# Kernel optimization log

Hardware: AMD Instinct MI355X
Metric: run time of the kernel (lower is better)

## Reference

```python
import jax, jax.numpy as jnp
import numpy as np

DIM = 2048
N_HEADS = 32
N_KV_HEADS = 8
HEAD_DIM = DIM // N_HEADS
N_REP = N_HEADS // N_KV_HEADS
BSZ, SEQ = 2, 2048


def setup_inputs() -> dict:
    key = jax.random.key(0)
    ks = jax.random.split(key, 6)
    hidden_states = jax.random.normal(ks[0], (BSZ, SEQ, DIM), jnp.float32)
    # additive causal mask [1,1,S,S]
    causal = jnp.tril(jnp.ones((SEQ, SEQ), jnp.bool_))
    attention_mask = jnp.where(causal, 0.0, -1e9).astype(jnp.float32)[None, None]
    # RoPE tables [S, head_dim]
    inv_freq = 1.0 / (10000.0 ** (np.arange(0, HEAD_DIM, 2, dtype=np.float32) / HEAD_DIM))
    t = np.arange(SEQ, dtype=np.float32)
    freqs = np.outer(t, inv_freq)  # [S, head_dim/2]
    emb = np.concatenate([freqs, freqs], axis=-1)  # [S, head_dim]
    position_cos = jnp.asarray(np.cos(emb), jnp.float32)
    position_sin = jnp.asarray(np.sin(emb), jnp.float32)
    s = 0.02
    Wq = jax.random.normal(ks[1], (DIM, DIM), jnp.float32) * s
    Wk = jax.random.normal(ks[2], (N_KV_HEADS * HEAD_DIM, DIM), jnp.float32) * s
    Wv = jax.random.normal(ks[3], (N_KV_HEADS * HEAD_DIM, DIM), jnp.float32) * s
    Wo = jax.random.normal(ks[4], (DIM, DIM), jnp.float32) * s
    return {"hidden_states": hidden_states, "attention_mask": attention_mask,
            "position_cos": position_cos, "position_sin": position_sin,
            "Wq": Wq, "Wk": Wk, "Wv": Wv, "Wo": Wo}


def _rotate_half(x):
    x1, x2 = jnp.split(x, 2, axis=-1)
    return jnp.concatenate([-x2, x1], axis=-1)


def _apply_rope(x, cos, sin):
    # x: [b, h, s, d]; cos/sin: [s, d] broadcast over (b, h)
    return x * cos + _rotate_half(x) * sin


def reference(hidden_states, attention_mask, position_cos, position_sin, Wq, Wk, Wv, Wo):
    b, s, _ = hidden_states.shape
    q = jnp.einsum('bsd,ed->bse', hidden_states, Wq).reshape(b, s, N_HEADS, HEAD_DIM).transpose(0, 2, 1, 3)
    k = jnp.einsum('bsd,ed->bse', hidden_states, Wk).reshape(b, s, N_KV_HEADS, HEAD_DIM).transpose(0, 2, 1, 3)
    v = jnp.einsum('bsd,ed->bse', hidden_states, Wv).reshape(b, s, N_KV_HEADS, HEAD_DIM).transpose(0, 2, 1, 3)
    q = _apply_rope(q, position_cos, position_sin)
    k = _apply_rope(k, position_cos, position_sin)
    # GQA: group query heads over kv heads instead of physically repeating k/v
    qg = q.reshape(b, N_KV_HEADS, N_REP, s, HEAD_DIM)
    scores = jnp.einsum('bgrqd,bgkd->bgrqk', qg, k) * (1.0 / jnp.sqrt(jnp.float32(HEAD_DIM)))
    scores = scores + attention_mask[:, :, None, :s, :s]
    weights = jax.nn.softmax(scores.astype(jnp.float32), axis=-1).astype(q.dtype)
    attn = jnp.einsum('bgrqk,bgkd->bgrqd', weights, v)
    attn = attn.reshape(b, N_HEADS, s, HEAD_DIM).transpose(0, 2, 1, 3).reshape(b, s, DIM)
    out = jnp.einsum('bsd,ed->bse', attn, Wo)
    return out
```

## Files before the change

### kernel.cpp

```cpp
#include <hip/hip_runtime.h>
#include <math.h>

#define BSZ 2
#define SEQ 2048
#define DIM 2048
#define NH 32
#define NKV 8
#define HD 64
#define KVDIM 512

typedef short short8 __attribute__((ext_vector_type(8)));
typedef short short4v __attribute__((ext_vector_type(4)));
typedef float f32x4 __attribute__((ext_vector_type(4)));
typedef int i32x4 __attribute__((ext_vector_type(4)));

__device__ __forceinline__ short fbf(float x) {
    unsigned u = __float_as_uint(x);
    u = (u + 0x7fffu + ((u >> 16) & 1u)) >> 16;
    return (short)u;
}

#define AS1(p) ((const __attribute__((address_space(1))) void*)(p))
#define AS3(p) ((__attribute__((address_space(3))) void*)(p))

#if defined(__has_builtin)
#if __has_builtin(__builtin_amdgcn_permlane16_swap) && __has_builtin(__builtin_amdgcn_permlane32_swap)
#define HAVE_PERMLANE 1
#endif
#endif

__device__ __forceinline__ float redmax4(float x) {
#ifdef HAVE_PERMLANE
    {
        auto p = __builtin_amdgcn_permlane16_swap(__float_as_uint(x), __float_as_uint(x), false, false);
        x = fmaxf(__uint_as_float(p[0]), __uint_as_float(p[1]));
    }
    {
        auto p = __builtin_amdgcn_permlane32_swap(__float_as_uint(x), __float_as_uint(x), false, false);
        x = fmaxf(__uint_as_float(p[0]), __uint_as_float(p[1]));
    }
#else
    x = fmaxf(x, __shfl_xor(x, 16));
    x = fmaxf(x, __shfl_xor(x, 32));
#endif
    return x;
}
__device__ __forceinline__ float redsum4(float x) {
#ifdef HAVE_PERMLANE
    {
        auto p = __builtin_amdgcn_permlane16_swap(__float_as_uint(x), __float_as_uint(x), false, false);
        x = __uint_as_float(p[0]) + __uint_as_float(p[1]);
    }
    {
        auto p = __builtin_amdgcn_permlane32_swap(__float_as_uint(x), __float_as_uint(x), false, false);
        x = __uint_as_float(p[0]) + __uint_as_float(p[1]);
    }
#else
    x += __shfl_xor(x, 16);
    x += __shfl_xor(x, 32);
#endif
    return x;
}

__global__ __launch_bounds__(256) void prep(const float* __restrict__ X,
                                            const float* __restrict__ Wq,
                                            const float* __restrict__ Wk,
                                            const float* __restrict__ Wv,
                                            const float* __restrict__ Wo,
                                            short* __restrict__ Xb,
                                            short* __restrict__ Wqkv,
                                            short* __restrict__ Wob) {
    int i = blockIdx.x * 256 + threadIdx.x;
    const float* src; short* dst; int j;
    if (i < 2097152)      { src = X;  dst = Xb;             j = i; }
    else if (i < 3145728) { src = Wq; dst = Wqkv;           j = i - 2097152; }
    else if (i < 3407872) { src = Wk; dst = Wqkv + 4194304; j = i - 3145728; }
    else if (i < 3670016) { src = Wv; dst = Wqkv + 5242880; j = i - 3407872; }
    else                  { src = Wo; dst = Wob;            j = i - 3670016; }
    float4 f = ((const float4*)src)[j];
    short4v s = { fbf(f.x), fbf(f.y), fbf(f.z), fbf(f.w) };
    ((short4v*)dst)[j] = s;
}

__global__ __launch_bounds__(512, 2) void gemm_qkv(const short* __restrict__ A,
                                                   const short* __restrict__ W,
                                                   const float* __restrict__ cosT,
                                                   const float* __restrict__ sinT,
                                                   short* __restrict__ Qo,
                                                   short* __restrict__ Ko,
                                                   short* __restrict__ Vo) {
    __shared__ short SM[65536];
    const int K = 2048;
    const int NT = 64;
    const int tid = threadIdx.x;
    const int lane = tid & 63, wave = tid >> 6;
    const int l15 = lane & 15, quad = lane >> 4;
    const int wm = (wave >> 2) * 128;
    const int wn = (wave & 3) * 64;
    const int orig = blockIdx.x;
    const int wgid = (orig & 7) * 24 + (orig >> 3);
    const int by = wgid / 12, bx = wgid - by * 12;
    const int m0 = by * 256, n0 = bx * 256;

    size_t aoff[2], boff[2]; int lslot[2];
#pragma unroll
    for (int v = 0; v < 2; ++v) {
        int s = v * 512 + tid;
        int pr = s >> 3, w = s & 7;
        int row = (pr << 1) | (w & 1);
        int c = (w >> 1) ^ (pr & 3);
        aoff[v] = (size_t)(m0 + row) * K + c * 8;
        boff[v] = (size_t)(n0 + row) * K + c * 8;
        lslot[v] = s * 8;
    }
    const int r0a = wm + l15;
    const int pa = r0a >> 1;
    const int slotA0 = pa * 8 + (((quad ^ (pa & 3)) << 1) | (r0a & 1));
    const int r0b = wn + l15;
    const int pb = r0b >> 1;
    const int slotB0 = pb * 8 + (((quad ^ (pb & 3)) << 1) | (r0b & 1));

    f32x4 acc[8][4] = {};

    auto issue = [&](int t) {
        const int kb = t * 32;
        short* Ad = SM + (t & 3) * 8192;
        short* Bd = SM + 32768 + (t & 3) * 8192;
#pragma unroll
        for (int v = 0; v < 2; ++v) {
            __builtin_amdgcn_global_load_lds(AS1(A + aoff[v] + kb), AS3(Ad + lslot[v]), 16, 0, 0);
            __builtin_amdgcn_global_load_lds(AS1(W + boff[v] + kb), AS3(Bd + lslot[v]), 16, 0, 0);
        }
    };
    issue(0); issue(1); issue(2);
    asm volatile("s_waitcnt vmcnt(8)" ::: "memory");
    __builtin_amdgcn_s_barrier();
    asm volatile("" ::: "memory");
    __builtin_amdgcn_sched_barrier(0);

    for (int t = 0; t < NT; ++t) {
        if (t < NT - 3) issue(t + 3);
        const short* Ab = SM + (t & 3) * 8192;
        const short* Bb = SM + 32768 + (t & 3) * 8192;
        short8 af[8], bf8[4];
#pragma unroll
        for (int j = 0; j < 4; ++j)
            bf8[j] = *(const short8*)&Bb[(slotB0 + j * 64) * 8];
#pragma unroll
        for (int i = 0; i < 8; ++i)
            af[i] = *(const short8*)&Ab[(slotA0 + i * 64) * 8];
        __builtin_amdgcn_s_setprio(1);
#pragma unroll
        for (int i = 0; i < 8; ++i)
#pragma unroll
            for (int j = 0; j < 4; ++j)
                acc[i][j] = __builtin_amdgcn_mfma_f32_16x16x32_bf16(af[i], bf8[j], acc[i][j], 0, 0, 0);
        __builtin_amdgcn_s_setprio(0);
        if (t < NT - 3)       asm volatile("s_waitcnt vmcnt(8)" ::: "memory");
        else if (t == NT - 3) asm volatile("s_waitcnt vmcnt(4)" ::: "memory");
        else if (t == NT - 2) asm volatile("s_waitcnt vmcnt(0)" ::: "memory");
        __builtin_amdgcn_s_barrier();
        asm volatile("" ::: "memory");
        __builtin_amdgcn_sched_barrier(0);
    }

    const int n0r = n0 + wn;
    if (n0r < 2560) {
        short* dst; int heads, hh; float scale;
        if (n0r < 2048) { dst = Qo; heads = NH;  hh = n0r >> 6;          scale = 0.125f * 1.44269504088896f; }
        else            { dst = Ko; heads = NKV; hh = (n0r - 2048) >> 6; scale = 1.0f; }
        short* EB = SM + wave * 8192;
#pragma unroll
        for (int i = 0; i < 8; ++i)
#pragma unroll
            for (int r = 0; r < 4; ++r) {
                int rr = i * 16 + quad * 4 + r;
                int s = (m0 + wm + rr) & (SEQ - 1);
                int msk = ((rr >> 1) & 7) * 8;
#pragma unroll
                for (int jp = 0; jp < 2; ++jp) {
                    int d1 = jp * 16 + l15;
                    float c1 = cosT[s * HD + d1], s1v = sinT[s * HD + d1];
                    float x1 = acc[i][jp][r], x2 = acc[i][jp + 2][r];
                    EB[rr * 64 + (d1 ^ msk)]        = fbf((x1 * c1 - x2 * s1v) * scale);
                    EB[rr * 64 + ((d1 + 32) ^ msk)] = fbf((x2 * c1 + x1 * s1v) * scale);
                }
            }
#pragma unroll
        for (int t = 0; t < 16; ++t) {
            int rr = (lane >> 3) + t * 8;
            int c = lane & 7;
            short8 v8 = *(const short8*)&EB[rr * 64 + c * 8];
            int dchunk = c ^ ((rr >> 1) & 7);
            int mrow = m0 + wm + rr;
            int s = mrow & (SEQ - 1), bb = mrow >> 11;
            *(short8*)&dst[((size_t)(bb * SEQ + s) * heads + hh) * HD + dchunk * 8] = v8;
        }
    } else {
        const int hh = (n0r - 2560) >> 6;
#pragma unroll
        for (int i = 0; i < 8; ++i) {
            int mrow4 = m0 + wm + i * 16 + quad * 4;
            int s_abs = mrow4 & (SEQ - 1);
            int bb = mrow4 >> 11;
            int blk = s_abs >> 6, kk = s_abs & 63;
            int ob = ((kk >> 5) << 3) | (((kk >> 2) & 3) << 1) | ((kk >> 4) & 1);
#pragma unroll
            for (int j = 0; j < 4; ++j) {
                int d = j * 16 + l15;
                short4v pk = { fbf(acc[i][j][0]), fbf(acc[i][j][1]),
                               fbf(acc[i][j][2]), fbf(acc[i][j][3]) };
                *(short4v*)&Vo[(((size_t)(bb * NKV + hh) * HD + d) * SEQ) + blk * 64 + ob * 4] = pk;
            }
        }
    }
}

__global__ __launch_bounds__(256) void gemm_bf16(const short* __restrict__ A,
                                                 const short* __restrict__ W,
                                                 float* __restrict__ C,
                                                 int M, int N, int K) {
    __shared__ short As[128 * 64];
    __shared__ short Bs[128 * 64];
    const int tid = threadIdx.x;
    const int lane = tid & 63, wave = tid >> 6;
    const int l15 = lane & 15, quad = lane >> 4;
    const int m0 = blockIdx.y * 128, n0 = blockIdx.x * 128;
    const int wm = (wave >> 1) * 64, wn = (wave & 1) * 64;
    f32x4 acc[4][4] = {};
    int srow[4], gcol[4];
#pragma unroll
    for (int v = 0; v < 4; ++v) {
        int s = v * 256 + tid;
        srow[v] = s >> 3;
        gcol[v] = ((s & 7) ^ (srow[v] & 7)) * 8;
    }
    for (int kb = 0; kb < K; kb += 64) {
        __syncthreads();
#pragma unroll
        for (int v = 0; v < 4; ++v) {
            int s = v * 256 + tid;
            __builtin_amdgcn_global_load_lds(AS1(A + (size_t)(m0 + srow[v]) * K + kb + gcol[v]),
                                             AS3(&As[s * 8]), 16, 0, 0);
            __builtin_amdgcn_global_load_lds(AS1(W + (size_t)(n0 + srow[v]) * K + kb + gcol[v]),
                                             AS3(&Bs[s * 8]), 16, 0, 0);
        }
        __syncthreads();
#pragma unroll
        for (int kh = 0; kh < 2; ++kh) {
            const int cs = ((kh * 4 + quad) ^ (l15 & 7)) * 8;
            short8 af[4], bf8[4];
#pragma unroll
            for (int i = 0; i < 4; ++i)
                af[i] = *(const short8*)&As[(wm + i * 16 + l15) * 64 + cs];
#pragma unroll
            for (int j = 0; j < 4; ++j)
                bf8[j] = *(const short8*)&Bs[(wn + j * 16 + l15) * 64 + cs];
#pragma unroll
            for (int i = 0; i < 4; ++i)
#pragma unroll
                for (int j = 0; j < 4; ++j)
                    acc[i][j] = __builtin_amdgcn_mfma_f32_16x16x32_bf16(af[i], bf8[j], acc[i][j], 0, 0, 0);
        }
    }
#pragma unroll
    for (int i = 0; i < 4; ++i)
#pragma unroll
        for (int j = 0; j < 4; ++j)
#pragma unroll
            for (int r = 0; r < 4; ++r)
                C[(size_t)(m0 + wm + i * 16 + quad * 4 + r) * N + n0 + wn + j * 16 + l15] = acc[i][j][r];
}

__global__ __launch_bounds__(512, 4) void flash4(const short* __restrict__ Qb,
                                                 const short* __restrict__ Kb,
                                                 const short* __restrict__ VT,
                                                 short* __restrict__ O) {
    __shared__ short Ks[2][128 * 64];
    __shared__ short Vs[2][64 * 128];
    const int d = blockIdx.x + blockIdx.y * 64;
    const int bh = (d & 255) >> 2;
    const int qt = (d < 256) ? 7 - (d & 3) : (d & 3);
    const int b = bh >> 5, h = bh & 31, kvh = h >> 2;
    const int tid = threadIdx.x;
    const int wave = tid >> 6, lane = tid & 63;
    const int l15 = lane & 15, quad = lane >> 4;

    short8 qf[2][2];
#pragma unroll
    for (int g = 0; g < 2; ++g) {
        const short* qp = Qb + ((size_t)b * SEQ + qt * 256 + g * 128 + wave * 16 + l15) * DIM + h * HD + quad * 8;
        qf[g][0] = *(const short8*)qp;
        qf[g][1] = *(const short8*)(qp + 32);
    }
    f32x4 o[2][4] = {};
    float m[2] = {-1e30f, -1e30f}, l[2] = {0.f, 0.f};

    const short* Kbase = Kb + (size_t)b * SEQ * KVDIM + kvh * HD;
    const short* Vbase = VT + (size_t)(b * NKV + kvh) * HD * SEQ;

    int krow[2], kcol[2], vrow[2], vcol[2];
#pragma unroll
    for (int v = 0; v < 2; ++v) {
        int s = v * 512 + tid;
        krow[v] = s >> 3;
        kcol[v] = ((s & 7) ^ (krow[v] & 7)) * 8;
        vrow[v] = s >> 4;
        vcol[v] = ((s & 15) ^ (vrow[v] & 7)) * 8;
    }
    auto issue = [&](int kt, int bi) {
#pragma unroll
        for (int v = 0; v < 2; ++v) {
            int s = v * 512 + tid;
            __builtin_amdgcn_global_load_lds(AS1(Kbase + (size_t)(kt * 128 + krow[v]) * KVDIM + kcol[v]),
                                             AS3(&Ks[bi][s * 8]), 16, 0, 0);
            __builtin_amdgcn_global_load_lds(AS1(Vbase + (size_t)vrow[v] * SEQ + kt * 128 + vcol[v]),
                                             AS3(&Vs[bi][s * 8]), 16, 0, 0);
        }
    };
    issue(0, 0);
    const int nkt = 2 * qt + 2;
    for (int kt = 0; kt < nkt; ++kt) {
        const int bi = kt & 1;
        __syncthreads();
        if (kt + 1 < nkt) issue(kt + 1, bi ^ 1);

#pragma unroll
        for (int g = 0; g < 2; ++g) {
            const int qmin = qt * 256 + g * 128 + wave * 16;
            if (kt * 128 > qmin + 15) continue;
            f32x4 st[8] = {};
#pragma unroll
            for (int kh = 0; kh < 2; ++kh) {
                const int cs = ((kh * 4 + quad) ^ (l15 & 7)) * 8;
#pragma unroll
                for (int nt = 0; nt < 8; ++nt) {
                    short8 ka = *(const short8*)&Ks[bi][(nt * 16 + l15) * 64 + cs];
                    st[nt] = __builtin_amdgcn_mfma_f32_16x16x32_bf16(ka, qf[g][kh], st[nt], 0, 0, 0);
                }
            }
            if (kt * 128 + 127 > qmin) {
                const int q = qmin + l15;
#pragma unroll
                for (int nt = 0; nt < 8; ++nt)
                    if (kt * 128 + nt * 16 + 15 > qmin) {
#pragma unroll
                        for (int r = 0; r < 4; ++r)
                            if (kt * 128 + nt * 16 + quad * 4 + r > q) st[nt][r] = -1e30f;
                    }
            }
            float mnt[8];
#pragma unroll
            for (int nt = 0; nt < 8; ++nt)
                mnt[nt] = fmaxf(fmaxf(fmaxf(st[nt][0], st[nt][1]), st[nt][2]), st[nt][3]);
            float ma = fmaxf(fmaxf(mnt[0], mnt[1]), mnt[2]);
            float mb = fmaxf(fmaxf(mnt[3], mnt[4]), mnt[5]);
            float mc = fmaxf(fmaxf(mnt[6], mnt[7]), ma);
            float mx = redmax4(fmaxf(mb, mc));

            const bool noskip = !__all(mx <= m[g]);
            float mn = m[g];
            float al = 1.0f;
            float alr[4];
            if (noskip) {
                mn = fmaxf(m[g], mx);
                al = __builtin_amdgcn_exp2f(m[g] - mn);
                m[g] = mn;
#pragma unroll
                for (int r = 0; r < 4; ++r) alr[r] = __shfl(al, quad * 4 + r);
            }
            i32x4 aw[4];
            f32x4 rs4 = {};
#pragma unroll
            for (int nt = 0; nt < 8; ++nt) {
                f32x4 pv;
#pragma unroll
                for (int r = 0; r < 4; ++r) pv[r] = __builtin_amdgcn_exp2f(st[nt][r] - mn);
                rs4 += pv;
                unsigned u0 = __float_as_uint(pv[0]) + 0x8000u;
                unsigned u1 = __float_as_uint(pv[1]) + 0x8000u;
                unsigned u2 = __float_as_uint(pv[2]) + 0x8000u;
                unsigned u3 = __float_as_uint(pv[3]) + 0x8000u;
                aw[nt >> 1][(nt & 1) * 2 + 0] = (int)__builtin_amdgcn_perm(u1, u0, 0x07060302u);
                aw[nt >> 1][(nt & 1) * 2 + 1] = (int)__builtin_amdgcn_perm(u3, u2, 0x07060302u);
            }
            float rs = redsum4((rs4[0] + rs4[1]) + (rs4[2] + rs4[3]));
            l[g] = l[g] * al + rs;
            if (noskip) {
#pragma unroll
                for (int dt = 0; dt < 4; ++dt) {
                    o[g][dt][0] *= alr[0]; o[g][dt][1] *= alr[1];
                    o[g][dt][2] *= alr[2]; o[g][dt][3] *= alr[3];
                }
            }
#pragma unroll
            for (int dt = 0; dt < 4; ++dt) {
                f32x4 t = o[g][dt];
#pragma unroll
                for (int kh = 0; kh < 4; ++kh) {
                    const int slot = (kh * 4 + quad) ^ (l15 & 7);
                    short8 vf = *(const short8*)&Vs[bi][(dt * 16 + l15) * 128 + slot * 8];
                    t = __builtin_amdgcn_mfma_f32_16x16x32_bf16(__builtin_bit_cast(short8, aw[kh]), vf, t, 0, 0, 0);
                }
                o[g][dt] = t;
            }
        }
    }
#pragma unroll
    for (int g = 0; g < 2; ++g) {
        float li = 1.0f / l[g];
        float lr[4];
#pragma unroll
        for (int r = 0; r < 4; ++r) lr[r] = __shfl(li, quad * 4 + r);
        short* Oo = O + ((size_t)b * SEQ + qt * 256 + g * 128 + wave * 16 + quad * 4) * DIM + h * HD + l15;
#pragma unroll
        for (int r = 0; r < 4; ++r)
#pragma unroll
            for (int dt = 0; dt < 4; ++dt)
                Oo[(size_t)r * DIM + dt * 16] = fbf(o[g][dt][r] * lr[r]);
    }
}

extern "C" void kernel_launch(void* const* d_in, const int* in_sizes, int n_in,
                              void* d_out, int out_size, void* d_ws, size_t ws_size,
                              hipStream_t stream) {
    const float* X    = (const float*)d_in[0];
    const float* cosT = (const float*)d_in[2];
    const float* sinT = (const float*)d_in[3];
    const float* Wq   = (const float*)d_in[4];
    const float* Wk   = (const float*)d_in[5];
    const float* Wv   = (const float*)d_in[6];
    const float* Wo   = (const float*)d_in[7];

    char* ws = (char*)d_ws;
    short* Xb    = (short*)(ws);
    short* ATTb  = Xb;
    short* WQKVb = (short*)(ws + 16777216);
    short* Wob   = (short*)(ws + 29360128);
    short* Qbb   = (short*)(ws + 37748736);
    short* Kbb   = (short*)(ws + 54525952);
    short* VTb   = (short*)(ws + 58720256);

    const int M = BSZ * SEQ;
    dim3 blk(256);

    prep<<<dim3(18432), blk, 0, stream>>>(X, Wq, Wk, Wv, Wo, Xb, WQKVb, Wob);
    gemm_qkv<<<dim3(192), dim3(512), 0, stream>>>(Xb, WQKVb, cosT, sinT, Qbb, Kbb, VTb);
    flash4<<<dim3(64, 8), dim3(512), 0, stream>>>(Qbb, Kbb, VTb, ATTb);
    gemm_bf16<<<dim3(DIM / 128, M / 128), blk, 0, stream>>>(ATTb, Wob, (float*)d_out, M, DIM, DIM);
}
```

Measured before the change: 307.5 us.

## Pipeline output GEMM with 4-stage LDS ring and shrink flash attention tiles

The output-projection GEMM now runs 512 threads on 256x128 tiles. It uses a 4-deep ring of K=32 LDS buffers with explicit vmcnt waits, a single barrier per step, setprio around the MFMA blocks, and a remapped workgroup id for L2 locality. The flash attention kernel drops to 128 query rows and 64-key tiles per block, which doubles the grid to 1024 blocks. It also swaps __syncthreads for manual barriers and waitcnts and adds setprio. The goal is to hide global load latency and improve load balance, at the cost of more blocks that each reload the K/V tiles and hand-tuned waitcnt accounting.

```diff
diff --git a/kernel.cpp b/kernel.cpp
--- a/kernel.cpp
+++ b/kernel.cpp
@@ -216,52 +216,89 @@
     }
 }
 
-__global__ __launch_bounds__(256) void gemm_bf16(const short* __restrict__ A,
-                                                 const short* __restrict__ W,
-                                                 float* __restrict__ C,
-                                                 int M, int N, int K) {
-    __shared__ short As[128 * 64];
-    __shared__ short Bs[128 * 64];
+__global__ __launch_bounds__(512, 2) void gemm_bf16(const short* __restrict__ A,
+                                                    const short* __restrict__ W,
+                                                    float* __restrict__ C,
+                                                    int M, int N, int K) {
+    __shared__ short SM[49152];
+    const int NT = K >> 5;
     const int tid = threadIdx.x;
     const int lane = tid & 63, wave = tid >> 6;
     const int l15 = lane & 15, quad = lane >> 4;
-    const int m0 = blockIdx.y * 128, n0 = blockIdx.x * 128;
-    const int wm = (wave >> 1) * 64, wn = (wave & 1) * 64;
+    const int wm = (wave >> 1) * 64;
+    const int wn = (wave & 1) * 64;
+    const int orig = blockIdx.x;
+    const int wgid = (orig & 7) * 32 + (orig >> 3);
+    const int by = wgid >> 4, bx = wgid & 15;
+    const int m0 = by * 256, n0 = bx * 128;
+
+    size_t aoff[2]; int lslotA[2];
+#pragma unroll
+    for (int v = 0; v < 2; ++v) {
+        int s = v * 512 + tid;
+        int pr = s >> 3, w = s & 7;
+        int row = (pr << 1) | (w & 1);
+        int c = (w >> 1) ^ (pr & 3);
+        aoff[v] = (size_t)(m0 + row) * K + c * 8;
+        lslotA[v] = s * 8;
+    }
+    size_t boff; int lslotB;
+    {
+        int s = tid;
+        int pr = s >> 3, w = s & 7;
+        int row = (pr << 1) | (w & 1);
+        int c = (w >> 1) ^ (pr & 3);
+        boff = (size_t)(n0 + row) * K + c * 8;
+        lslotB = s * 8;
+    }
+    const int r0a = wm + l15;
+    const int pa = r0a >> 1;
+    const int slotA0 = pa * 8 + (((quad ^ (pa & 3)) << 1) | (r0a & 1));
+    const int r0b = wn + l15;
+    const int pb = r0b >> 1;
+    const int slotB0 = pb * 8 + (((quad ^ (pb & 3)) << 1) | (r0b & 1));
+
     f32x4 acc[4][4] = {};
-    int srow[4], gcol[4];
-#pragma unroll
-    for (int v = 0; v < 4; ++v) {
-        int s = v * 256 + tid;
-        srow[v] = s >> 3;
-        gcol[v] = ((s & 7) ^ (srow[v] & 7)) * 8;
-    }
-    for (int kb = 0; kb < K; kb += 64) {
-        __syncthreads();
-#pragma unroll
-        for (int v = 0; v < 4; ++v) {
-            int s = v * 256 + tid;
-            __builtin_amdgcn_global_load_lds(AS1(A + (size_t)(m0 + srow[v]) * K + kb + gcol[v]),
-                                             AS3(&As[s * 8]), 16, 0, 0);
-            __builtin_amdgcn_global_load_lds(AS1(W + (size_t)(n0 + srow[v]) * K + kb + gcol[v]),
-                                             AS3(&Bs[s * 8]), 16, 0, 0);
-        }
-        __syncthreads();
-#pragma unroll
-        for (int kh = 0; kh < 2; ++kh) {
-            const int cs = ((kh * 4 + quad) ^ (l15 & 7)) * 8;
-            short8 af[4], bf8[4];
-#pragma unroll
-            for (int i = 0; i < 4; ++i)
-                af[i] = *(const short8*)&As[(wm + i * 16 + l15) * 64 + cs];
+
+    auto issue = [&](int t) {
+        const int kb = t * 32;
+        short* Ad = SM + (t & 3) * 8192;
+        short* Bd = SM + 32768 + (t & 3) * 4096;
+#pragma unroll
+        for (int v = 0; v < 2; ++v)
+            __builtin_amdgcn_global_load_lds(AS1(A + aoff[v] + kb), AS3(Ad + lslotA[v]), 16, 0, 0);
+        __builtin_amdgcn_global_load_lds(AS1(W + boff + kb), AS3(Bd + lslotB), 16, 0, 0);
+    };
+    issue(0); issue(1); issue(2);
+    asm volatile("s_waitcnt vmcnt(6)" ::: "memory");
+    __builtin_amdgcn_s_barrier();
+    asm volatile("" ::: "memory");
+    __builtin_amdgcn_sched_barrier(0);
+
+    for (int t = 0; t < NT; ++t) {
+        if (t < NT - 3) issue(t + 3);
+        const short* Ab = SM + (t & 3) * 8192;
+        const short* Bb = SM + 32768 + (t & 3) * 4096;
+        short8 af[4], bf8[4];
+#pragma unroll
+        for (int j = 0; j < 4; ++j)
+            bf8[j] = *(const short8*)&Bb[(slotB0 + j * 64) * 8];
+#pragma unroll
+        for (int i = 0; i < 4; ++i)
+            af[i] = *(const short8*)&Ab[(slotA0 + i * 64) * 8];
+        __builtin_amdgcn_s_setprio(1);
+#pragma unroll
+        for (int i = 0; i < 4; ++i)
 #pragma unroll
             for (int j = 0; j < 4; ++j)
-                bf8[j] = *(const short8*)&Bs[(wn + j * 16 + l15) * 64 + cs];
-#pragma unroll
-            for (int i = 0; i < 4; ++i)
-#pragma unroll
-                for (int j = 0; j < 4; ++j)
-                    acc[i][j] = __builtin_amdgcn_mfma_f32_16x16x32_bf16(af[i], bf8[j], acc[i][j], 0, 0, 0);
-        }
+                acc[i][j] = __builtin_amdgcn_mfma_f32_16x16x32_bf16(af[i], bf8[j], acc[i][j], 0, 0, 0);
+        __builtin_amdgcn_s_setprio(0);
+        if (t < NT - 3)       asm volatile("s_waitcnt vmcnt(6)" ::: "memory");
+        else if (t == NT - 3) asm volatile("s_waitcnt vmcnt(3)" ::: "memory");
+        else if (t == NT - 2) asm volatile("s_waitcnt vmcnt(0)" ::: "memory");
+        __builtin_amdgcn_s_barrier();
+        asm volatile("" ::: "memory");
+        __builtin_amdgcn_sched_barrier(0);
     }
 #pragma unroll
     for (int i = 0; i < 4; ++i)
@@ -276,149 +313,137 @@
                                                  const short* __restrict__ Kb,
                                                  const short* __restrict__ VT,
                                                  short* __restrict__ O) {
-    __shared__ short Ks[2][128 * 64];
-    __shared__ short Vs[2][64 * 128];
-    const int d = blockIdx.x + blockIdx.y * 64;
-    const int bh = (d & 255) >> 2;
-    const int qt = (d < 256) ? 7 - (d & 3) : (d & 3);
+    __shared__ short Ks[2][64 * 64];
+    __shared__ short Vs[2][64 * 64];
+    const int d = blockIdx.x;
+    const int bh = (d & 511) >> 3;
+    const int qt = (d < 512) ? 15 - (d & 7) : (d & 7);
     const int b = bh >> 5, h = bh & 31, kvh = h >> 2;
     const int tid = threadIdx.x;
     const int wave = tid >> 6, lane = tid & 63;
     const int l15 = lane & 15, quad = lane >> 4;
 
-    short8 qf[2][2];
-#pragma unroll
-    for (int g = 0; g < 2; ++g) {
-        const short* qp = Qb + ((size_t)b * SEQ + qt * 256 + g * 128 + wave * 16 + l15) * DIM + h * HD + quad * 8;
-        qf[g][0] = *(const short8*)qp;
-        qf[g][1] = *(const short8*)(qp + 32);
-    }
-    f32x4 o[2][4] = {};
-    float m[2] = {-1e30f, -1e30f}, l[2] = {0.f, 0.f};
+    const short* qp = Qb + ((size_t)b * SEQ + qt * 128 + wave * 16 + l15) * DIM + h * HD + quad * 8;
+    short8 qf0 = *(const short8*)qp;
+    short8 qf1 = *(const short8*)(qp + 32);
+
+    f32x4 o[4] = {};
+    float m = -1e30f, l = 0.f;
 
     const short* Kbase = Kb + (size_t)b * SEQ * KVDIM + kvh * HD;
     const short* Vbase = VT + (size_t)(b * NKV + kvh) * HD * SEQ;
 
-    int krow[2], kcol[2], vrow[2], vcol[2];
-#pragma unroll
-    for (int v = 0; v < 2; ++v) {
-        int s = v * 512 + tid;
-        krow[v] = s >> 3;
-        kcol[v] = ((s & 7) ^ (krow[v] & 7)) * 8;
-        vrow[v] = s >> 4;
-        vcol[v] = ((s & 15) ^ (vrow[v] & 7)) * 8;
-    }
+    const int srow = tid >> 3;
+    const int scol = ((tid & 7) ^ (srow & 7)) * 8;
     auto issue = [&](int kt, int bi) {
-#pragma unroll
-        for (int v = 0; v < 2; ++v) {
-            int s = v * 512 + tid;
-            __builtin_amdgcn_global_load_lds(AS1(Kbase + (size_t)(kt * 128 + krow[v]) * KVDIM + kcol[v]),
-                                             AS3(&Ks[bi][s * 8]), 16, 0, 0);
-            __builtin_amdgcn_global_load_lds(AS1(Vbase + (size_t)vrow[v] * SEQ + kt * 128 + vcol[v]),
-                                             AS3(&Vs[bi][s * 8]), 16, 0, 0);
-        }
+        __builtin_amdgcn_global_load_lds(AS1(Kbase + (size_t)(kt * 64 + srow) * KVDIM + scol),
+                                         AS3(&Ks[bi][tid * 8]), 16, 0, 0);
+        __builtin_amdgcn_global_load_lds(AS1(Vbase + (size_t)srow * SEQ + kt * 64 + scol),
+                                         AS3(&Vs[bi][tid * 8]), 16, 0, 0);
     };
     issue(0, 0);
     const int nkt = 2 * qt + 2;
+    const int qmin = qt * 128 + wave * 16;
     for (int kt = 0; kt < nkt; ++kt) {
         const int bi = kt & 1;
-        __syncthreads();
-        if (kt + 1 < nkt) issue(kt + 1, bi ^ 1);
-
-#pragma unroll
-        for (int g = 0; g < 2; ++g) {
-            const int qmin = qt * 256 + g * 128 + wave * 16;
-            if (kt * 128 > qmin + 15) continue;
-            f32x4 st[8] = {};
+        __builtin_amdgcn_s_barrier();
+        asm volatile("" ::: "memory");
+        if (kt + 1 < nkt) {
+            issue(kt + 1, bi ^ 1);
+            asm volatile("s_waitcnt vmcnt(2)" ::: "memory");
+        } else {
+            asm volatile("s_waitcnt vmcnt(0)" ::: "memory");
+        }
+        __builtin_amdgcn_sched_barrier(0);
+        if (kt * 64 > qmin + 15) continue;
+
+        f32x4 st[4] = {};
+        __builtin_amdgcn_s_setprio(1);
+#pragma unroll
+        for (int kh = 0; kh < 2; ++kh) {
+            const int cs = ((kh * 4 + quad) ^ (l15 & 7)) * 8;
+#pragma unroll
+            for (int nt = 0; nt < 4; ++nt) {
+                short8 ka = *(const short8*)&Ks[bi][(nt * 16 + l15) * 64 + cs];
+                st[nt] = __builtin_amdgcn_mfma_f32_16x16x32_bf16(ka, kh ? qf1 : qf0, st[nt], 0, 0, 0);
+            }
+        }
+        __builtin_amdgcn_s_setprio(0);
+        if (kt * 64 + 63 > qmin) {
+            const int q = qmin + l15;
+#pragma unroll
+            for (int nt = 0; nt < 4; ++nt)
+                if (kt * 64 + nt * 16 + 15 > qmin) {
+#pragma unroll
+                    for (int r = 0; r < 4; ++r)
+                        if (kt * 64 + nt * 16 + quad * 4 + r > q) st[nt][r] = -1e30f;
+                }
+        }
+        float mnt[4];
+#pragma unroll
+        for (int nt = 0; nt < 4; ++nt)
+            mnt[nt] = fmaxf(fmaxf(fmaxf(st[nt][0], st[nt][1]), st[nt][2]), st[nt][3]);
+        float mx = redmax4(fmaxf(fmaxf(mnt[0], mnt[1]), fmaxf(mnt[2], mnt[3])));
+
+        const bool noskip = !__all(mx <= m);
+        float mn = m;
+        float al = 1.0f;
+        float alr[4];
+        if (noskip) {
+            mn = fmaxf(m, mx);
+            al = __builtin_amdgcn_exp2f(m - mn);
+            m = mn;
+#pragma unroll
+            for (int r = 0; r < 4; ++r) alr[r] = __shfl(al, quad * 4 + r);
+        }
+        i32x4 aw[2];
+        f32x4 rs4 = {};
+#pragma unroll
+        for (int nt = 0; nt < 4; ++nt) {
+            f32x4 pv;
+#pragma unroll
+            for (int r = 0; r < 4; ++r) pv[r] = __builtin_amdgcn_exp2f(st[nt][r] - mn);
+            rs4 += pv;
+            unsigned u0 = __float_as_uint(pv[0]) + 0x8000u;
+            unsigned u1 = __float_as_uint(pv[1]) + 0x8000u;
+            unsigned u2 = __float_as_uint(pv[2]) + 0x8000u;
+            unsigned u3 = __float_as_uint(pv[3]) + 0x8000u;
+            aw[nt >> 1][(nt & 1) * 2 + 0] = (int)__builtin_amdgcn_perm(u1, u0, 0x07060302u);
+            aw[nt >> 1][(nt & 1) * 2 + 1] = (int)__builtin_amdgcn_perm(u3, u2, 0x07060302u);
+        }
+        float rs = redsum4((rs4[0] + rs4[1]) + (rs4[2] + rs4[3]));
+        l = l * al + rs;
+        if (noskip) {
+#pragma unroll
+            for (int dt = 0; dt < 4; ++dt) {
+                o[dt][0] *= alr[0]; o[dt][1] *= alr[1];
+                o[dt][2] *= alr[2]; o[dt][3] *= alr[3];
+            }
+        }
+        __builtin_amdgcn_s_setprio(1);
+#pragma unroll
+        for (int dt = 0; dt < 4; ++dt) {
+            f32x4 t = o[dt];
 #pragma unroll
             for (int kh = 0; kh < 2; ++kh) {
-                const int cs = ((kh * 4 + quad) ^ (l15 & 7)) * 8;
-#pragma unroll
-                for (int nt = 0; nt < 8; ++nt) {
-                    short8 ka = *(const short8*)&Ks[bi][(nt * 16 + l15) * 64 + cs];
-                    st[nt] = __builtin_amdgcn_mfma_f32_16x16x32_bf16(ka, qf[g][kh], st[nt], 0, 0, 0);
-                }
+                const int slot = (kh * 4 + quad) ^ (l15 & 7);
+                short8 vf = *(const short8*)&Vs[bi][(dt * 16 + l15) * 64 + slot * 8];
+                t = __builtin_amdgcn_mfma_f32_16x16x32_bf16(__builtin_bit_cast(short8, aw[kh]), vf, t, 0, 0, 0);
             }
-            if (kt * 128 + 127 > qmin) {
-                const int q = qmin + l15;
-#pragma unroll
-                for (int nt = 0; nt < 8; ++nt)
-                    if (kt * 128 + nt * 16 + 15 > qmin) {
-#pragma unroll
-                        for (int r = 0; r < 4; ++r)
-                            if (kt * 128 + nt * 16 + quad * 4 + r > q) st[nt][r] = -1e30f;
-                    }
-            }
-            float mnt[8];
-#pragma unroll
-            for (int nt = 0; nt < 8; ++nt)
-                mnt[nt] = fmaxf(fmaxf(fmaxf(st[nt][0], st[nt][1]), st[nt][2]), st[nt][3]);
-            float ma = fmaxf(fmaxf(mnt[0], mnt[1]), mnt[2]);
-            float mb = fmaxf(fmaxf(mnt[3], mnt[4]), mnt[5]);
-            float mc = fmaxf(fmaxf(mnt[6], mnt[7]), ma);
-            float mx = redmax4(fmaxf(mb, mc));
-
-            const bool noskip = !__all(mx <= m[g]);
-            float mn = m[g];
-            float al = 1.0f;
-            float alr[4];
-            if (noskip) {
-                mn = fmaxf(m[g], mx);
-                al = __builtin_amdgcn_exp2f(m[g] - mn);
-                m[g] = mn;
-#pragma unroll
-                for (int r = 0; r < 4; ++r) alr[r] = __shfl(al, quad * 4 + r);
-            }
-            i32x4 aw[4];
-            f32x4 rs4 = {};
-#pragma unroll
-            for (int nt = 0; nt < 8; ++nt) {
-                f32x4 pv;
-#pragma unroll
-                for (int r = 0; r < 4; ++r) pv[r] = __builtin_amdgcn_exp2f(st[nt][r] - mn);
-                rs4 += pv;
-                unsigned u0 = __float_as_uint(pv[0]) + 0x8000u;
-                unsigned u1 = __float_as_uint(pv[1]) + 0x8000u;
-                unsigned u2 = __float_as_uint(pv[2]) + 0x8000u;
-                unsigned u3 = __float_as_uint(pv[3]) + 0x8000u;
-                aw[nt >> 1][(nt & 1) * 2 + 0] = (int)__builtin_amdgcn_perm(u1, u0, 0x07060302u);
-                aw[nt >> 1][(nt & 1) * 2 + 1] = (int)__builtin_amdgcn_perm(u3, u2, 0x07060302u);
-            }
-            float rs = redsum4((rs4[0] + rs4[1]) + (rs4[2] + rs4[3]));
-            l[g] = l[g] * al + rs;
-            if (noskip) {
-#pragma unroll
-                for (int dt = 0; dt < 4; ++dt) {
-                    o[g][dt][0] *= alr[0]; o[g][dt][1] *= alr[1];
-                    o[g][dt][2] *= alr[2]; o[g][dt][3] *= alr[3];
-                }
-            }
-#pragma unroll
-            for (int dt = 0; dt < 4; ++dt) {
-                f32x4 t = o[g][dt];
-#pragma unroll
-                for (int kh = 0; kh < 4; ++kh) {
-                    const int slot = (kh * 4 + quad) ^ (l15 & 7);
-                    short8 vf = *(const short8*)&Vs[bi][(dt * 16 + l15) * 128 + slot * 8];
-                    t = __builtin_amdgcn_mfma_f32_16x16x32_bf16(__builtin_bit_cast(short8, aw[kh]), vf, t, 0, 0, 0);
-                }
-                o[g][dt] = t;
-            }
-        }
-    }
-#pragma unroll
-    for (int g = 0; g < 2; ++g) {
-        float li = 1.0f / l[g];
-        float lr[4];
-#pragma unroll
-        for (int r = 0; r < 4; ++r) lr[r] = __shfl(li, quad * 4 + r);
-        short* Oo = O + ((size_t)b * SEQ + qt * 256 + g * 128 + wave * 16 + quad * 4) * DIM + h * HD + l15;
-#pragma unroll
-        for (int r = 0; r < 4; ++r)
-#pragma unroll
-            for (int dt = 0; dt < 4; ++dt)
-                Oo[(size_t)r * DIM + dt * 16] = fbf(o[g][dt][r] * lr[r]);
-    }
+            o[dt] = t;
+        }
+        __builtin_amdgcn_s_setprio(0);
+    }
+    float li = 1.0f / l;
+    float lr[4];
+#pragma unroll
+    for (int r = 0; r < 4; ++r) lr[r] = __shfl(li, quad * 4 + r);
+    short* Oo = O + ((size_t)b * SEQ + qt * 128 + wave * 16 + quad * 4) * DIM + h * HD + l15;
+#pragma unroll
+    for (int r = 0; r < 4; ++r)
+#pragma unroll
+        for (int dt = 0; dt < 4; ++dt)
+            Oo[(size_t)r * DIM + dt * 16] = fbf(o[dt][r] * lr[r]);
 }
 
 extern "C" void kernel_launch(void* const* d_in, const int* in_sizes, int n_in,
@@ -442,10 +467,9 @@
     short* VTb   = (short*)(ws + 58720256);
 
     const int M = BSZ * SEQ;
-    dim3 blk(256);
-
-    prep<<<dim3(18432), blk, 0, stream>>>(X, Wq, Wk, Wv, Wo, Xb, WQKVb, Wob);
+
+    prep<<<dim3(18432), dim3(256), 0, stream>>>(X, Wq, Wk, Wv, Wo, Xb, WQKVb, Wob);
     gemm_qkv<<<dim3(192), dim3(512), 0, stream>>>(Xb, WQKVb, cosT, sinT, Qbb, Kbb, VTb);
-    flash4<<<dim3(64, 8), dim3(512), 0, stream>>>(Qbb, Kbb, VTb, ATTb);
-    gemm_bf16<<<dim3(DIM / 128, M / 128), blk, 0, stream>>>(ATTb, Wob, (float*)d_out, M, DIM, DIM);
-}
+    flash4<<<dim3(1024), dim3(512), 0, stream>>>(Qbb, Kbb, VTb, ATTb);
+    gemm_bf16<<<dim3(256), dim3(512), 0, stream>>>(ATTb, Wob, (float*)d_out, M, DIM, DIM);
+}
```

Result: faster. 291.1 us (-5.3%).
